# Performance work log

Measured on AMD Instinct MI355X. Metric: run time of the kernel, lower is better.

The kernel has to match this reference:

```python
import jax, jax.numpy as jnp
import numpy as np

N, E, D_IN, D_OUT = 100000, 1600000, 64, 64


def setup_inputs() -> dict:
    key = jax.random.key(0)
    k0, k1, k2, k3 = jax.random.split(key, 4)
    x = jax.random.normal(k0, (N, D_IN), dtype=jnp.float32)
    edge_index = jax.random.randint(k1, (2, E), 0, N)  # [2, E] (src, dst)
    W = jax.random.normal(k2, (D_IN, D_OUT), dtype=jnp.float32) / np.sqrt(D_IN).astype(np.float32)
    b = jnp.zeros((D_OUT,), dtype=jnp.float32)
    causal_attention = jax.random.normal(k3, (D_OUT, D_OUT), dtype=jnp.float32)
    return {"x": x, "edge_index": edge_index, "W": W, "b": b,
            "causal_attention": causal_attention, "L": 1}


def gcn_conv(x, edge_index, W, b):
    # PyG GCNConv: x' = D^{-1/2} (A + I) D^{-1/2} (x W) + b
    n = x.shape[0]
    xw = x @ W  # [N, D_OUT]
    loops = jnp.arange(n)
    src = jnp.concatenate([edge_index[0], loops])  # [E+N]
    dst = jnp.concatenate([edge_index[1], loops])
    deg = jax.ops.segment_sum(jnp.ones_like(src, dtype=xw.dtype), dst, num_segments=n)
    dinv = jnp.where(deg > 0, jax.lax.rsqrt(deg), 0.0)
    norm = dinv[src] * dinv[dst]  # [E+N]
    agg = jax.ops.segment_sum(norm[:, None] * xw[src], dst, num_segments=n)  # [N, D_OUT]
    return agg + b


def reference(x, edge_index, W, b, causal_attention, L):
    x_conv = gcn_conv(x, edge_index, W, b)
    causal_weights = jax.nn.softmax(causal_attention, axis=1)  # row softmax
    return x_conv @ causal_weights  # [N, D_OUT]
```

## Files before the change

### kernel.cpp

```cpp
#include <hip/hip_runtime.h>
#include <hip/hip_bf16.h>


#define D 64
#define BSHIFT 6
#define BNODES 64
#define ARENA_CAP 1728
#define BIN_TILE 8192

__device__ __forceinline__ unsigned short f2bf(float f) {
    union { float f; unsigned int u; } c;
    c.f = f;
    unsigned int u = c.u;
    u += 0x7fffu + ((u >> 16) & 1u);
    return (unsigned short)(u >> 16);
}
__device__ __forceinline__ float bflo(unsigned int u) {
    union { unsigned int u; float f; } c;
    c.u = u << 16;
    return c.f;
}
__device__ __forceinline__ float bfhi(unsigned int u) {
    union { unsigned int u; float f; } c;
    c.u = u & 0xffff0000u;
    return c.f;
}

__global__ __launch_bounds__(256) void prep_kernel(const float* __restrict__ W,
                                                   const float* __restrict__ b,
                                                   const float* __restrict__ A,
                                                   float* __restrict__ M,
                                                   float* __restrict__ bs,
                                                   int* __restrict__ cursor, int nbuck) {
    __shared__ float S[D * D];
    int t = threadIdx.x;
    int gidx = blockIdx.x * 256 + t;
    if (gidx < nbuck) cursor[gidx] = gidx * ARENA_CAP;
    int wv = t >> 6, lane = t & 63;
#pragma unroll 4
    for (int rr = 0; rr < 16; rr++) {
        int r = wv * 16 + rr;
        float a = A[r * D + lane];
        float m = a;
        for (int off = 32; off; off >>= 1) m = fmaxf(m, __shfl_xor(m, off));
        float p = __expf(a - m);
        float ssum = p;
        for (int off = 32; off; off >>= 1) ssum += __shfl_xor(ssum, off);
        S[r * D + lane] = p / ssum;
    }
    __syncthreads();
    int k = blockIdx.x * 4 + wv;
    float acc = 0.f;
    for (int d2 = 0; d2 < D; d2++) acc += W[k * D + d2] * S[d2 * D + lane];
    M[k * D + lane] = acc;
    if (blockIdx.x == 0 && t < D) {
        float a2 = 0.f;
        for (int d2 = 0; d2 < D; d2++) a2 += b[d2] * S[d2 * D + t];
        bs[t] = a2;
    }
}

__global__ __launch_bounds__(512) void bin_kernel(const int* __restrict__ src,
                                                  const int* __restrict__ dst,
                                                  int* __restrict__ cursor,
                                                  int* __restrict__ binned, int E) {
    __shared__ int h[2048];
    int t = threadIdx.x;
    for (int i = t; i < 2048; i += 512) h[i] = 0;
    __syncthreads();
    int base = blockIdx.x * BIN_TILE;
    int pv[16], bk[16], rv[16];
#pragma unroll
    for (int k = 0; k < 16; k++) {
        int e = base + k * 512 + t;
        if (e < E) {
            int s = src[e], d = dst[e];
            bk[k] = (d >> BSHIFT) & 2047;
            pv[k] = (s << BSHIFT) | (d & (BNODES - 1));
            rv[k] = atomicAdd(&h[bk[k]], 1);
        }
    }
    __syncthreads();
    for (int b2 = t; b2 < 2048; b2 += 512) {
        int c = h[b2];
        if (c) h[b2] = atomicAdd(&cursor[b2], c);
    }
    __syncthreads();
#pragma unroll
    for (int k = 0; k < 16; k++) {
        int e = base + k * 512 + t;
        if (e < E) binned[h[bk[k]] + rv[k]] = pv[k];
    }
}

__global__ __launch_bounds__(256) void dk_kernel(const int* __restrict__ binned,
                                                 const int* __restrict__ cursor,
                                                 float* __restrict__ dinv, int N) {
    __shared__ int h[BNODES];
    int t = threadIdx.x;
    int b = blockIdx.x;
    int base = b * ARENA_CAP;
    int cnt = cursor[b] - base;
    if (cnt > ARENA_CAP) cnt = ARENA_CAP;
    if (t < BNODES) h[t] = 0;
    __syncthreads();
    for (int i = t; i < cnt; i += 256)
        atomicAdd(&h[binned[base + i] & (BNODES - 1)], 1);
    __syncthreads();
    if (t < BNODES) {
        int node = (b << BSHIFT) + t;
        if (node < N) dinv[node] = rsqrtf((float)(h[t] + 1));
    }
}

__device__ __forceinline__ void fma4(float4& a, float xv, const float4& m) {
    a.x += xv * m.x; a.y += xv * m.y; a.z += xv * m.z; a.w += xv * m.w;
}
__global__ __launch_bounds__(256) void zmat_kernel(const float* __restrict__ x,
                                                   const float* __restrict__ M,
                                                   const float* __restrict__ dinv,
                                                   unsigned short* __restrict__ zbf,
                                                   int N) {
    __shared__ float Ms[D * D];
    __shared__ float xs[64][D + 4];
    int t = threadIdx.x;
    int row0 = blockIdx.x << 6;
    for (int i = t; i < (D * D) / 4; i += 256)
        ((float4*)Ms)[i] = ((const float4*)M)[i];
    for (int w = t; w < 1024; w += 256) {
        int r = w >> 4, c4 = (w & 15) << 2;
        int row = row0 + r;
        float4 v = make_float4(0.f, 0.f, 0.f, 0.f);
        if (row < N) v = *(const float4*)&x[(size_t)row * D + c4];
        *(float4*)&xs[r][c4] = v;
    }
    __syncthreads();
    int cg = t & 15, rg = t >> 4;
    int r0 = rg << 2, c0 = cg << 2;
    float4 a0 = make_float4(0.f, 0.f, 0.f, 0.f);
    float4 a1 = a0, a2 = a0, a3 = a0;
#pragma unroll 4
    for (int k = 0; k < D; k += 4) {
        float4 x0 = *(const float4*)&xs[r0 + 0][k];
        float4 x1 = *(const float4*)&xs[r0 + 1][k];
        float4 x2 = *(const float4*)&xs[r0 + 2][k];
        float4 x3 = *(const float4*)&xs[r0 + 3][k];
        float4 m0 = *(const float4*)&Ms[(k + 0) * D + c0];
        float4 m1 = *(const float4*)&Ms[(k + 1) * D + c0];
        float4 m2 = *(const float4*)&Ms[(k + 2) * D + c0];
        float4 m3 = *(const float4*)&Ms[(k + 3) * D + c0];
        fma4(a0, x0.x, m0); fma4(a0, x0.y, m1); fma4(a0, x0.z, m2); fma4(a0, x0.w, m3);
        fma4(a1, x1.x, m0); fma4(a1, x1.y, m1); fma4(a1, x1.z, m2); fma4(a1, x1.w, m3);
        fma4(a2, x2.x, m0); fma4(a2, x2.y, m1); fma4(a2, x2.z, m2); fma4(a2, x2.w, m3);
        fma4(a3, x3.x, m0); fma4(a3, x3.y, m1); fma4(a3, x3.z, m2); fma4(a3, x3.w, m3);
    }
    int rowb = row0 + r0;
    if (rowb < N) {
        float4 dv4 = *(const float4*)&dinv[rowb];
        ushort4 s0, s1, s2, s3;
        s0.x = f2bf(dv4.x * a0.x); s0.y = f2bf(dv4.x * a0.y);
        s0.z = f2bf(dv4.x * a0.z); s0.w = f2bf(dv4.x * a0.w);
        s1.x = f2bf(dv4.y * a1.x); s1.y = f2bf(dv4.y * a1.y);
        s1.z = f2bf(dv4.y * a1.z); s1.w = f2bf(dv4.y * a1.w);
        s2.x = f2bf(dv4.z * a2.x); s2.y = f2bf(dv4.z * a2.y);
        s2.z = f2bf(dv4.z * a2.z); s2.w = f2bf(dv4.z * a2.w);
        s3.x = f2bf(dv4.w * a3.x); s3.y = f2bf(dv4.w * a3.y);
        s3.z = f2bf(dv4.w * a3.z); s3.w = f2bf(dv4.w * a3.w);
        *(ushort4*)&zbf[(size_t)(rowb + 0) * D + c0] = s0;
        *(ushort4*)&zbf[(size_t)(rowb + 1) * D + c0] = s1;
        *(ushort4*)&zbf[(size_t)(rowb + 2) * D + c0] = s2;
        *(ushort4*)&zbf[(size_t)(rowb + 3) * D + c0] = s3;
    }
}

__global__ __launch_bounds__(256) void sg_kernel(const unsigned short* __restrict__ zbf,
                                                 const int* __restrict__ binned,
                                                 const int* __restrict__ cursor,
                                                 const float* __restrict__ bs,
                                                 float* __restrict__ out, int N) {
    __shared__ int buf[ARENA_CAP];
    __shared__ int srt[ARENA_CAP];
    __shared__ int h[BNODES];
    __shared__ int cur[BNODES];
    __shared__ int rs[BNODES];
    __shared__ float dv[BNODES];
    int t = threadIdx.x;
    int b = blockIdx.x;
    int base = b * ARENA_CAP;
    int cnt = cursor[b] - base;
    if (cnt > ARENA_CAP) cnt = ARENA_CAP;
    if (t < BNODES) h[t] = 0;
    __syncthreads();
    for (int i = t; i < cnt; i += 256) {
        int p = binned[base + i];
        buf[i] = p;
        atomicAdd(&h[p & (BNODES - 1)], 1);
    }
    __syncthreads();
    if (t < BNODES) {
        int v = h[t];
        int sc = v;
#pragma unroll
        for (int off = 1; off < BNODES; off <<= 1) {
            int u = __shfl_up(sc, off);
            if (t >= off) sc += u;
        }
        rs[t] = sc - v;
        cur[t] = sc - v;
        dv[t] = rsqrtf((float)(v + 1));
    }
    __syncthreads();
    for (int i = t; i < cnt; i += 256) {
        int p = buf[i];
        int pos = atomicAdd(&cur[p & (BNODES - 1)], 1);
        srt[pos] = (int)((unsigned)p >> BSHIFT);
    }
    __syncthreads();

    int lane = t & 63, wv = t >> 6;
    int qg = lane >> 4;
    int c4 = lane & 15;
    float4 bb = ((const float4*)bs)[c4];
#pragma unroll 1
    for (int nl = 0; nl < 16; nl++) {
        int ln = wv * 16 + nl;
        int node = (b << BSHIFT) + ln;
        int s = rs[ln];
        int deg = h[ln];
        float a0 = 0.f, a1 = 0.f, a2 = 0.f, a3 = 0.f;
        int k = 0;
        for (; k + 15 < deg; k += 16) {
            int p0 = srt[s + k + qg];
            int p1 = srt[s + k + 4 + qg];
            int p2 = srt[s + k + 8 + qg];
            int p3 = srt[s + k + 12 + qg];
            uint2 u0 = *(const uint2*)&zbf[(size_t)p0 * D + 4 * c4];
            uint2 u1 = *(const uint2*)&zbf[(size_t)p1 * D + 4 * c4];
            uint2 u2 = *(const uint2*)&zbf[(size_t)p2 * D + 4 * c4];
            uint2 u3 = *(const uint2*)&zbf[(size_t)p3 * D + 4 * c4];
            a0 += bflo(u0.x); a1 += bfhi(u0.x); a2 += bflo(u0.y); a3 += bfhi(u0.y);
            a0 += bflo(u1.x); a1 += bfhi(u1.x); a2 += bflo(u1.y); a3 += bfhi(u1.y);
            a0 += bflo(u2.x); a1 += bfhi(u2.x); a2 += bflo(u2.y); a3 += bfhi(u2.y);
            a0 += bflo(u3.x); a1 += bfhi(u3.x); a2 += bflo(u3.y); a3 += bfhi(u3.y);
        }
        for (; k + 7 < deg; k += 8) {
            int p0 = srt[s + k + qg];
            int p1 = srt[s + k + 4 + qg];
            uint2 u0 = *(const uint2*)&zbf[(size_t)p0 * D + 4 * c4];
            uint2 u1 = *(const uint2*)&zbf[(size_t)p1 * D + 4 * c4];
            a0 += bflo(u0.x); a1 += bfhi(u0.x); a2 += bflo(u0.y); a3 += bfhi(u0.y);
            a0 += bflo(u1.x); a1 += bfhi(u1.x); a2 += bflo(u1.y); a3 += bfhi(u1.y);
        }
        for (; k + 3 < deg; k += 4) {
            int p0 = srt[s + k + qg];
            uint2 u0 = *(const uint2*)&zbf[(size_t)p0 * D + 4 * c4];
            a0 += bflo(u0.x); a1 += bfhi(u0.x); a2 += bflo(u0.y); a3 += bfhi(u0.y);
        }
        int r = deg - k;
        if (r) {
            int p0 = srt[s + k + (qg < r ? qg : 0)];
            uint2 u0 = *(const uint2*)&zbf[(size_t)p0 * D + 4 * c4];
            if (qg < r) {
                a0 += bflo(u0.x); a1 += bfhi(u0.x);
                a2 += bflo(u0.y); a3 += bfhi(u0.y);
            }
        }
        a0 += __shfl_xor(a0, 16); a1 += __shfl_xor(a1, 16);
        a2 += __shfl_xor(a2, 16); a3 += __shfl_xor(a3, 16);
        a0 += __shfl_xor(a0, 32); a1 += __shfl_xor(a1, 32);
        a2 += __shfl_xor(a2, 32); a3 += __shfl_xor(a3, 32);
        if (lane < 16 && node < N) {
            uint2 uz = *(const uint2*)&zbf[(size_t)node * D + 4 * c4];
            float di = dv[ln];
            float4 o;
            o.x = di * (a0 + bflo(uz.x)) + bb.x;
            o.y = di * (a1 + bfhi(uz.x)) + bb.y;
            o.z = di * (a2 + bflo(uz.y)) + bb.z;
            o.w = di * (a3 + bfhi(uz.y)) + bb.w;
            *(float4*)&out[(size_t)node * D + 4 * c4] = o;
        }
    }
}

extern "C" void kernel_launch(void* const* d_in, const int* in_sizes, int n_in,
                              void* d_out, int out_size, void* d_ws, size_t ws_size,
                              hipStream_t stream) {
    const float* x = (const float*)d_in[0];
    const int* ei = (const int*)d_in[1];
    const float* W = (const float*)d_in[2];
    const float* b = (const float*)d_in[3];
    const float* A = (const float*)d_in[4];

    const int N = in_sizes[0] / D;
    const int E = in_sizes[1] / 2;
    const int* src = ei;
    const int* dst = ei + E;
    const int NBUCK = (N + BNODES - 1) >> BSHIFT;

    char* ws = (char*)d_ws;
    size_t off = 0;
    auto alloc = [&](size_t bytes) -> char* {
        char* p = ws + off;
        off = (off + bytes + 255) & ~(size_t)255;
        return p;
    };
    int* cursor = (int*)alloc((size_t)NBUCK * 4);
    float* dinv = (float*)alloc((size_t)N * 4);
    float* M = (float*)alloc((size_t)D * D * 4);
    float* bs = (float*)alloc((size_t)D * 4);
    int* binned = (int*)alloc((size_t)NBUCK * ARENA_CAP * 4);
    unsigned short* zbf = (unsigned short*)alloc((size_t)N * D * 2);
    (void)ws_size;

    prep_kernel<<<16, 256, 0, stream>>>(W, b, A, M, bs, cursor, NBUCK);
    bin_kernel<<<(E + BIN_TILE - 1) / BIN_TILE, 512, 0, stream>>>(src, dst, cursor, binned, E);
    dk_kernel<<<NBUCK, 256, 0, stream>>>(binned, cursor, dinv, N);
    zmat_kernel<<<(N + 63) >> 6, 256, 0, stream>>>(x, M, dinv, zbf, N);
    sg_kernel<<<NBUCK, 256, 0, stream>>>(zbf, binned, cursor, bs, (float*)d_out, N);
}
```

Before: 167.9 us.

## Fuse degree counting into zmat kernel and widen bin kernel blocks

Removes the separate dk_kernel and its dinv buffer. The degree histogram per 64-node bucket is now computed inside zmat_kernel, which uses the same bucket-to-row mapping. zmat drops to 128 threads with 8 rows per thread and reads M straight from global memory instead of staging it in LDS, and bin_kernel moves to 1024 threads with 8 items each. This saves one launch and one global round trip for dinv, but zmat now also reads the binned arena and holds more registers per thread.

```diff
diff --git a/kernel.cpp b/kernel.cpp
--- a/kernel.cpp
+++ b/kernel.cpp
@@ -60,19 +60,19 @@
     }
 }
 
-__global__ __launch_bounds__(512) void bin_kernel(const int* __restrict__ src,
-                                                  const int* __restrict__ dst,
-                                                  int* __restrict__ cursor,
-                                                  int* __restrict__ binned, int E) {
+__global__ __launch_bounds__(1024) void bin_kernel(const int* __restrict__ src,
+                                                   const int* __restrict__ dst,
+                                                   int* __restrict__ cursor,
+                                                   int* __restrict__ binned, int E) {
     __shared__ int h[2048];
     int t = threadIdx.x;
-    for (int i = t; i < 2048; i += 512) h[i] = 0;
+    for (int i = t; i < 2048; i += 1024) h[i] = 0;
     __syncthreads();
     int base = blockIdx.x * BIN_TILE;
-    int pv[16], bk[16], rv[16];
-#pragma unroll
-    for (int k = 0; k < 16; k++) {
-        int e = base + k * 512 + t;
+    int pv[8], bk[8], rv[8];
+#pragma unroll
+    for (int k = 0; k < 8; k++) {
+        int e = base + k * 1024 + t;
         if (e < E) {
             int s = src[e], d = dst[e];
             bk[k] = (d >> BSHIFT) & 2047;
@@ -81,53 +81,40 @@
         }
     }
     __syncthreads();
-    for (int b2 = t; b2 < 2048; b2 += 512) {
+    for (int b2 = t; b2 < 2048; b2 += 1024) {
         int c = h[b2];
         if (c) h[b2] = atomicAdd(&cursor[b2], c);
     }
     __syncthreads();
 #pragma unroll
-    for (int k = 0; k < 16; k++) {
-        int e = base + k * 512 + t;
+    for (int k = 0; k < 8; k++) {
+        int e = base + k * 1024 + t;
         if (e < E) binned[h[bk[k]] + rv[k]] = pv[k];
     }
 }
 
-__global__ __launch_bounds__(256) void dk_kernel(const int* __restrict__ binned,
-                                                 const int* __restrict__ cursor,
-                                                 float* __restrict__ dinv, int N) {
+__device__ __forceinline__ void fma4(float4& a, float xv, const float4& m) {
+    a.x += xv * m.x; a.y += xv * m.y; a.z += xv * m.z; a.w += xv * m.w;
+}
+__global__ __launch_bounds__(128) void zmat_kernel(const float* __restrict__ x,
+                                                   const float* __restrict__ M,
+                                                   const int* __restrict__ binned,
+                                                   const int* __restrict__ cursor,
+                                                   unsigned short* __restrict__ zbf,
+                                                   int N) {
+    __shared__ float xs[64][D + 4];
     __shared__ int h[BNODES];
     int t = threadIdx.x;
     int b = blockIdx.x;
-    int base = b * ARENA_CAP;
-    int cnt = cursor[b] - base;
+    int row0 = b << 6;
+    if (t < BNODES) h[t] = 0;
+    __syncthreads();
+    int abase = b * ARENA_CAP;
+    int cnt = cursor[b] - abase;
     if (cnt > ARENA_CAP) cnt = ARENA_CAP;
-    if (t < BNODES) h[t] = 0;
-    __syncthreads();
-    for (int i = t; i < cnt; i += 256)
-        atomicAdd(&h[binned[base + i] & (BNODES - 1)], 1);
-    __syncthreads();
-    if (t < BNODES) {
-        int node = (b << BSHIFT) + t;
-        if (node < N) dinv[node] = rsqrtf((float)(h[t] + 1));
-    }
-}
-
-__device__ __forceinline__ void fma4(float4& a, float xv, const float4& m) {
-    a.x += xv * m.x; a.y += xv * m.y; a.z += xv * m.z; a.w += xv * m.w;
-}
-__global__ __launch_bounds__(256) void zmat_kernel(const float* __restrict__ x,
-                                                   const float* __restrict__ M,
-                                                   const float* __restrict__ dinv,
-                                                   unsigned short* __restrict__ zbf,
-                                                   int N) {
-    __shared__ float Ms[D * D];
-    __shared__ float xs[64][D + 4];
-    int t = threadIdx.x;
-    int row0 = blockIdx.x << 6;
-    for (int i = t; i < (D * D) / 4; i += 256)
-        ((float4*)Ms)[i] = ((const float4*)M)[i];
-    for (int w = t; w < 1024; w += 256) {
+    for (int i = t; i < cnt; i += 128)
+        atomicAdd(&h[binned[abase + i] & (BNODES - 1)], 1);
+    for (int w = t; w < 1024; w += 128) {
         int r = w >> 4, c4 = (w & 15) << 2;
         int row = row0 + r;
         float4 v = make_float4(0.f, 0.f, 0.f, 0.f);
@@ -136,40 +123,37 @@
     }
     __syncthreads();
     int cg = t & 15, rg = t >> 4;
-    int r0 = rg << 2, c0 = cg << 2;
-    float4 a0 = make_float4(0.f, 0.f, 0.f, 0.f);
-    float4 a1 = a0, a2 = a0, a3 = a0;
-#pragma unroll 4
+    int r0 = rg << 3, c0 = cg << 2;
+    float4 acc[8];
+#pragma unroll
+    for (int rr = 0; rr < 8; rr++) acc[rr] = make_float4(0.f, 0.f, 0.f, 0.f);
+#pragma unroll 2
     for (int k = 0; k < D; k += 4) {
-        float4 x0 = *(const float4*)&xs[r0 + 0][k];
-        float4 x1 = *(const float4*)&xs[r0 + 1][k];
-        float4 x2 = *(const float4*)&xs[r0 + 2][k];
-        float4 x3 = *(const float4*)&xs[r0 + 3][k];
-        float4 m0 = *(const float4*)&Ms[(k + 0) * D + c0];
-        float4 m1 = *(const float4*)&Ms[(k + 1) * D + c0];
-        float4 m2 = *(const float4*)&Ms[(k + 2) * D + c0];
-        float4 m3 = *(const float4*)&Ms[(k + 3) * D + c0];
-        fma4(a0, x0.x, m0); fma4(a0, x0.y, m1); fma4(a0, x0.z, m2); fma4(a0, x0.w, m3);
-        fma4(a1, x1.x, m0); fma4(a1, x1.y, m1); fma4(a1, x1.z, m2); fma4(a1, x1.w, m3);
-        fma4(a2, x2.x, m0); fma4(a2, x2.y, m1); fma4(a2, x2.z, m2); fma4(a2, x2.w, m3);
-        fma4(a3, x3.x, m0); fma4(a3, x3.y, m1); fma4(a3, x3.z, m2); fma4(a3, x3.w, m3);
-    }
-    int rowb = row0 + r0;
-    if (rowb < N) {
-        float4 dv4 = *(const float4*)&dinv[rowb];
-        ushort4 s0, s1, s2, s3;
-        s0.x = f2bf(dv4.x * a0.x); s0.y = f2bf(dv4.x * a0.y);
-        s0.z = f2bf(dv4.x * a0.z); s0.w = f2bf(dv4.x * a0.w);
-        s1.x = f2bf(dv4.y * a1.x); s1.y = f2bf(dv4.y * a1.y);
-        s1.z = f2bf(dv4.y * a1.z); s1.w = f2bf(dv4.y * a1.w);
-        s2.x = f2bf(dv4.z * a2.x); s2.y = f2bf(dv4.z * a2.y);
-        s2.z = f2bf(dv4.z * a2.z); s2.w = f2bf(dv4.z * a2.w);
-        s3.x = f2bf(dv4.w * a3.x); s3.y = f2bf(dv4.w * a3.y);
-        s3.z = f2bf(dv4.w * a3.z); s3.w = f2bf(dv4.w * a3.w);
-        *(ushort4*)&zbf[(size_t)(rowb + 0) * D + c0] = s0;
-        *(ushort4*)&zbf[(size_t)(rowb + 1) * D + c0] = s1;
-        *(ushort4*)&zbf[(size_t)(rowb + 2) * D + c0] = s2;
-        *(ushort4*)&zbf[(size_t)(rowb + 3) * D + c0] = s3;
+        float4 m0 = *(const float4*)&M[(k + 0) * D + c0];
+        float4 m1 = *(const float4*)&M[(k + 1) * D + c0];
+        float4 m2 = *(const float4*)&M[(k + 2) * D + c0];
+        float4 m3 = *(const float4*)&M[(k + 3) * D + c0];
+#pragma unroll
+        for (int rr = 0; rr < 8; rr++) {
+            float4 xv = *(const float4*)&xs[r0 + rr][k];
+            fma4(acc[rr], xv.x, m0);
+            fma4(acc[rr], xv.y, m1);
+            fma4(acc[rr], xv.z, m2);
+            fma4(acc[rr], xv.w, m3);
+        }
+    }
+#pragma unroll
+    for (int rr = 0; rr < 8; rr++) {
+        int row = row0 + r0 + rr;
+        if (row < N) {
+            float di = rsqrtf((float)(h[r0 + rr] + 1));
+            ushort4 s;
+            s.x = f2bf(di * acc[rr].x);
+            s.y = f2bf(di * acc[rr].y);
+            s.z = f2bf(di * acc[rr].z);
+            s.w = f2bf(di * acc[rr].w);
+            *(ushort4*)&zbf[(size_t)row * D + c0] = s;
+        }
     }
 }
 
@@ -305,7 +289,6 @@
         return p;
     };
     int* cursor = (int*)alloc((size_t)NBUCK * 4);
-    float* dinv = (float*)alloc((size_t)N * 4);
     float* M = (float*)alloc((size_t)D * D * 4);
     float* bs = (float*)alloc((size_t)D * 4);
     int* binned = (int*)alloc((size_t)NBUCK * ARENA_CAP * 4);
@@ -313,8 +296,7 @@
     (void)ws_size;
 
     prep_kernel<<<16, 256, 0, stream>>>(W, b, A, M, bs, cursor, NBUCK);
-    bin_kernel<<<(E + BIN_TILE - 1) / BIN_TILE, 512, 0, stream>>>(src, dst, cursor, binned, E);
-    dk_kernel<<<NBUCK, 256, 0, stream>>>(binned, cursor, dinv, N);
-    zmat_kernel<<<(N + 63) >> 6, 256, 0, stream>>>(x, M, dinv, zbf, N);
+    bin_kernel<<<(E + BIN_TILE - 1) / BIN_TILE, 1024, 0, stream>>>(src, dst, cursor, binned, E);
+    zmat_kernel<<<NBUCK, 128, 0, stream>>>(x, M, binned, cursor, zbf, N);
     sg_kernel<<<NBUCK, 256, 0, stream>>>(zbf, binned, cursor, bs, (float*)d_out, N);
 }
```

After: 167.4 us. About the same (-0.3%).
